# Kernel optimization log

Hardware: AMD Instinct MI355X
Metric: run time of the kernel (lower is better)

## Reference

```python
import jax, jax.numpy as jnp
import numpy as np

B, L, D_IN = 4, 2048, 80
D, H, DFF, WIN = 128, 16, 128, 64
DH = D // H
BN_EPS = 1e-5


def sinusoidal_positional_encoding(l, d, dtype):
    # Faithful to source: pos_j = 10000 ** (j / d) (exponent j/d, not 2j/d)
    n = d // 2 + (d % 2 == 1)
    pos_i = jnp.arange(l, dtype=dtype)[:, None]                  # [L,1]
    pos_j = jnp.power(jnp.asarray(10000.0, dtype), jnp.arange(n, dtype=dtype) / d)  # [n]
    ang = pos_i / pos_j                                          # [L,n]
    pos = jnp.stack([jnp.sin(ang), jnp.cos(ang)], axis=-1).reshape(l, -1)
    return pos[:, :d]                                            # [L,D]


def local_window_disallowed_mask(l, win):
    # Source: mask starts as ones (True = disallowed), zeros only strictly
    i = jnp.arange(l)
    diff = jnp.abs(i[:, None] - i[None, :])
    allowed = (diff >= 1) & (diff <= win)
    return ~allowed                                              # [L,L] bool, True = masked


def setup_inputs() -> dict:
    key = jax.random.key(0)
    ks = jax.random.split(key, 17)
    s = 0.05  # weight scale for numerical stability
    return {
        "x": jax.random.normal(ks[0], (B, L, D_IN), jnp.float32),
        "conv_w": jax.random.normal(ks[1], (D, D_IN), jnp.float32) * s,
        "conv_b": jax.random.normal(ks[2], (D,), jnp.float32) * s,
        "bn_g": jax.random.uniform(ks[3], (D,), jnp.float32, 0.5, 1.5),
        "bn_b": jax.random.normal(ks[4], (D,), jnp.float32) * s,
        "bn_rm": jax.random.normal(ks[5], (D,), jnp.float32) * s,
        "bn_rv": jax.random.uniform(ks[6], (D,), jnp.float32, 0.5, 1.5),
        "in_proj_w": jax.random.normal(ks[7], (3 * D, D), jnp.float32) * s,
        "in_proj_b": jax.random.normal(ks[8], (3 * D,), jnp.float32) * s,
        "out_w": jax.random.normal(ks[9], (D, D), jnp.float32) * s,
        "out_b": jax.random.normal(ks[10], (D,), jnp.float32) * s,
        "ff_w1": jax.random.normal(ks[11], (DFF, D), jnp.float32) * s,
        "ff_b1": jax.random.normal(ks[12], (DFF,), jnp.float32) * s,
        "ff_w2": jax.random.normal(ks[13], (D, DFF), jnp.float32) * s,
        "ff_b2": jax.random.normal(ks[14], (D,), jnp.float32) * s,
        "fc_w": jax.random.normal(ks[15], (D_IN, D), jnp.float32) * s,
        "fc_b": jax.random.normal(ks[16], (D_IN,), jnp.float32) * s,
    }


def _forward(x, conv_w, conv_b, bn_g, bn_b, bn_rm, bn_rv,
             in_proj_w, in_proj_b, out_w, out_b,
             ff_w1, ff_b1, ff_w2, ff_b2, fc_w, fc_b):
    b, l, _ = x.shape
    dt = x.dtype
    # Conv1d(kernel=1) + ReLU + BatchNorm1d (eval mode, running stats)
    h = jax.nn.relu(jnp.einsum('bli,oi->blo', x, conv_w) + conv_b)     # [B,L,D]
    h = (h - bn_rm) * (bn_g * jax.lax.rsqrt(bn_rv + BN_EPS)) + bn_b
    # positional encoding
    h = h + sinusoidal_positional_encoding(l, D, dt)
    # MultiheadAttention (torch semantics: joint in_proj, scaled dot, out_proj)
    qkv = jnp.einsum('bld,ed->ble', h, in_proj_w) + in_proj_b          # [B,L,3D]
    q, k, v = jnp.split(qkv, 3, axis=-1)
    q = q.reshape(b, l, H, DH).transpose(0, 2, 1, 3)                   # [B,H,L,dh]
    k = k.reshape(b, l, H, DH).transpose(0, 2, 1, 3)
    v = v.reshape(b, l, H, DH).transpose(0, 2, 1, 3)
    scores = jnp.einsum('bhqd,bhkd->bhqk', q, k) / jnp.sqrt(jnp.asarray(DH, dt))
    mask = local_window_disallowed_mask(l, WIN)                        # True = masked
    scores = jnp.where(mask, jnp.finfo(dt).min, scores)
    attn = jax.nn.softmax(scores, axis=-1)                             # [B,H,L,L]
    ctx = jnp.einsum('bhqk,bhkd->bhqd', attn, v)
    ctx = ctx.transpose(0, 2, 1, 3).reshape(b, l, D)
    attn_out = jnp.einsum('bld,od->blo', ctx, out_w) + out_b           # [B,L,D]
    # FFN (no residual in source)
    f = jax.nn.relu(jnp.einsum('bld,fd->blf', attn_out, ff_w1) + ff_b1)
    f = jnp.einsum('blf,df->bld', f, ff_w2) + ff_b2                    # [B,L,D]
    # final head
    return jnp.einsum('bld,od->blo', f, fc_w) + fc_b                   # [B,L,80]


def reference(x, conv_w, conv_b, bn_g, bn_b, bn_rm, bn_rv,
              in_proj_w, in_proj_b, out_w, out_b,
              ff_w1, ff_b1, ff_w2, ff_b2, fc_w, fc_b):
    return _forward(x, conv_w, conv_b, bn_g, bn_b, bn_rm, bn_rv,
                    in_proj_w, in_proj_b, out_w, out_b,
                    ff_w1, ff_b1, ff_w2, ff_b2, fc_w, fc_b)
```

## Files before the change

kernel.cpp:

```cpp
#include <hip/hip_runtime.h>
#include <math.h>

constexpr int L_ = 2048, D_ = 128, H_ = 16;
constexpr int T_ = 8192;
constexpr int DIN = 80;
constexpr int LDX = T_;
constexpr int BHL = 131072;

typedef __attribute__((ext_vector_type(8))) short short8;
typedef __attribute__((ext_vector_type(4))) float floatx4;

__device__ float g_xT  [DIN * T_];
__device__ float g_posT[D_ * L_];
__device__ unsigned short g_h_hi[T_ * D_];
__device__ unsigned short g_h_lo[T_ * D_];
__device__ unsigned short g_Wq_hi[3 * D_ * D_];
__device__ unsigned short g_Wq_lo[3 * D_ * D_];
__device__ float g_qkv [3 * D_ * T_];
__device__ float g_ctx [D_ * T_];
__device__ float g_f1  [D_ * T_];
__device__ float g_pA  [2 * 8 * BHL];
__device__ float g_pl  [2 * BHL];
__device__ float g_WconvT[DIN * D_];
__device__ float g_Wf1T  [D_ * D_];
__device__ float g_WfcT  [D_ * D_];
__device__ float g_bf1   [D_];
__device__ float g_bfc   [D_];

__device__ __forceinline__ unsigned short bf16h(float x) {
    unsigned u = __float_as_uint(x);
    return (unsigned short)((u + 0x7FFFu + ((u >> 16) & 1u)) >> 16);
}
__device__ __forceinline__ float bf16f(unsigned short h) {
    return __uint_as_float(((unsigned)h) << 16);
}

__global__ __launch_bounds__(256) void prep_kernel(
        const float* __restrict__ x,
        const float* __restrict__ conv_w,
        const float* __restrict__ in_proj_w,
        const float* __restrict__ out_w,  const float* __restrict__ out_b,
        const float* __restrict__ ff_w1,  const float* __restrict__ ff_b1,
        const float* __restrict__ ff_w2,  const float* __restrict__ ff_b2,
        const float* __restrict__ fc_w,   const float* __restrict__ fc_b) {
    __shared__ float smem[80 * 65];
    int bid = blockIdx.x, tid = threadIdx.x;

    if (bid < 128) {
        int t0 = bid * 64;
        for (int i = tid; i < 64 * 80; i += 256) {
            int t = i / 80, k = i - t * 80;
            smem[k * 65 + t] = x[(size_t)t0 * 80 + i];
        }
        __syncthreads();
        for (int i = tid; i < 80 * 64; i += 256) {
            int k = i >> 6, tt = i & 63;
            g_xT[(size_t)k * T_ + t0 + tt] = smem[k * 65 + tt];
        }
        return;
    }
    if (bid < 640) {
        int idx = (bid - 128) * 256 + tid;
        int l = idx >> 6, j = idx & 63;
        float inv = __expf((float)j * (-9.210340371976184f / 128.0f));
        float ang = (float)l * inv;
        g_posT[(2 * j) * L_ + l]     = sinf(ang);
        g_posT[(2 * j + 1) * L_ + l] = cosf(ang);
        return;
    }
    if (bid < 680) {
        int e = (bid - 640) * 256 + tid;
        int o = e / 80, k = e - o * 80;
        g_WconvT[k * D_ + o] = conv_w[e];
        return;
    }
    if (bid < 872) {
        int e = (bid - 680) * 256 + tid;
        float v = in_proj_w[e];
        unsigned short hi = bf16h(v);
        g_Wq_hi[e] = hi;
        g_Wq_lo[e] = bf16h(v - bf16f(hi));
        return;
    }
    float* rowbuf = smem;
    float* red = smem + 256;
    if (bid < 936) {
        int sub = tid >> 7, k = tid & 127;
        int f = (bid - 872) * 2 + sub;
        rowbuf[sub * 128 + k] = ff_w1[f * 128 + k];
        __syncthreads();
        float acc = 0.f;
#pragma unroll 8
        for (int o = 0; o < 128; o++)
            acc = fmaf(rowbuf[sub * 128 + o], out_w[o * 128 + k], acc);
        g_Wf1T[k * 128 + f] = acc;
        red[tid] = rowbuf[sub * 128 + k] * out_b[k];
        __syncthreads();
        for (int s = 64; s > 0; s >>= 1) {
            if (k < s) red[tid] += red[tid + s];
            __syncthreads();
        }
        if (k == 0) g_bf1[f] = red[sub * 128] + ff_b1[f];
        return;
    }
    {
        int sub = tid >> 7, k = tid & 127;
        int o = (bid - 936) * 2 + sub;
        rowbuf[sub * 128 + k] = (o < 80) ? fc_w[o * 128 + k] : 0.f;
        __syncthreads();
        float acc = 0.f;
#pragma unroll 8
        for (int d = 0; d < 128; d++)
            acc = fmaf(rowbuf[sub * 128 + d], ff_w2[d * 128 + k], acc);
        g_WfcT[k * 128 + o] = acc;
        red[tid] = rowbuf[sub * 128 + k] * ff_b2[k];
        __syncthreads();
        for (int s = 64; s > 0; s >>= 1) {
            if (k < s) red[tid] += red[tid + s];
            __syncthreads();
        }
        if (k == 0) g_bfc[o] = (o < 80) ? (red[sub * 128] + fc_b[o]) : 0.f;
        return;
    }
}

template <int K, int BK, int BN, int LDW, int EPI>
__global__ __launch_bounds__(256) void gemm_kernel(
        const float* __restrict__ X, const float* __restrict__ Wt,
        const float* __restrict__ bias,
        const float* __restrict__ bg, const float* __restrict__ bb,
        const float* __restrict__ brm, const float* __restrict__ brv,
        float* __restrict__ Y) {
    constexpr int TN = BN / 16;
    __shared__ float Xs[BK][64];
    __shared__ float Ws[BK][BN];
    int tid = threadIdx.x;
    int t0 = blockIdx.x * 64;
    int cb = blockIdx.y * BN;
    int tc = tid & 15, tr = tid >> 4;

    float acc[4][TN] = {};
    for (int kc = 0; kc < K; kc += BK) {
        for (int i = tid; i < BK * 16; i += 256) {
            int k = i >> 4, f = i & 15;
            *(float4*)&Xs[k][f * 4] =
                *(const float4*)&X[(size_t)(kc + k) * LDX + t0 + f * 4];
        }
        for (int i = tid; i < BK * (BN / 4); i += 256) {
            int k = i / (BN / 4), f = i - k * (BN / 4);
            *(float4*)&Ws[k][f * 4] =
                *(const float4*)&Wt[(size_t)(kc + k) * LDW + cb + f * 4];
        }
        __syncthreads();
#pragma unroll 4
        for (int k = 0; k < BK; ++k) {
            float4 a = *(float4*)&Xs[k][tr * 4];
            float av[4] = {a.x, a.y, a.z, a.w};
            float wv[TN];
#pragma unroll
            for (int jj = 0; jj < TN; jj++) wv[jj] = Ws[k][tc * TN + jj];
#pragma unroll
            for (int i = 0; i < 4; i++)
#pragma unroll
                for (int jj = 0; jj < TN; jj++)
                    acc[i][jj] = fmaf(av[i], wv[jj], acc[i][jj]);
        }
        __syncthreads();
    }

    if (EPI == 5) {
#pragma unroll
        for (int i = 0; i < 4; i++) {
            int t = t0 + tr * 4 + i;
            unsigned hi2 = 0, lo2 = 0;
#pragma unroll
            for (int jj = 0; jj < TN; jj++) {
                int c = cb + tc * TN + jj;
                float v = acc[i][jj] + bias[c];
                v = fmaxf(v, 0.0f);
                v = (v - brm[c]) * (bg[c] * rsqrtf(brv[c] + 1e-5f)) + bb[c];
                v += g_posT[c * L_ + (t & 2047)];
                unsigned short h = bf16h(v);
                float lo = v - bf16f(h);
                hi2 |= ((unsigned)h) << (16 * jj);
                lo2 |= ((unsigned)bf16h(lo)) << (16 * jj);
            }
            int cbase = cb + tc * TN;
            *(unsigned*)&g_h_hi[(size_t)t * 128 + cbase] = hi2;
            *(unsigned*)&g_h_lo[(size_t)t * 128 + cbase] = lo2;
        }
        return;
    }
    if (EPI == 4) {
#pragma unroll
        for (int jj = 0; jj < TN; jj++) {
            int c = cb + tc * TN + jj;
            if (c < 80) {
                float bv = bias[c];
#pragma unroll
                for (int i = 0; i < 4; i++) {
                    int t = t0 + tr * 4 + i;
                    Y[(size_t)t * 80 + c] = acc[i][jj] + bv;
                }
            }
        }
        return;
    }
#pragma unroll
    for (int jj = 0; jj < TN; jj++) {
        int c = cb + tc * TN + jj;
        float bv = bias[c];
        float vs[4];
#pragma unroll
        for (int i = 0; i < 4; i++) {
            float v = acc[i][jj] + bv;
            if (EPI == 1) v = fmaxf(v, 0.0f);
            vs[i] = v;
        }
        *(float4*)&Y[(size_t)c * LDX + t0 + tr * 4] = *(float4*)vs;
    }
}

__global__ __launch_bounds__(256) void qkv_mfma(const float* __restrict__ in_proj_b) {
    __shared__ unsigned short WsH[64 * 136];
    __shared__ unsigned short WsL[64 * 136];
    __shared__ unsigned short HsH[32 * 136];
    __shared__ unsigned short HsL[32 * 136];
    int tid = threadIdx.x;
    int t0 = blockIdx.x * 32;
    int cb = blockIdx.y * 64;

    for (int i = tid; i < 1024; i += 256) {
        int r = i >> 4, c8 = (i & 15) * 8;
        *(uint4*)&WsH[r * 136 + c8] = *(const uint4*)&g_Wq_hi[(size_t)(cb + r) * 128 + c8];
        *(uint4*)&WsL[r * 136 + c8] = *(const uint4*)&g_Wq_lo[(size_t)(cb + r) * 128 + c8];
    }
    for (int i = tid; i < 512; i += 256) {
        int r = i >> 4, c8 = (i & 15) * 8;
        *(uint4*)&HsH[r * 136 + c8] = *(const uint4*)&g_h_hi[(size_t)(t0 + r) * 128 + c8];
        *(uint4*)&HsL[r * 136 + c8] = *(const uint4*)&g_h_lo[(size_t)(t0 + r) * 128 + c8];
    }
    __syncthreads();

    int lane = tid & 63, w = tid >> 6;
    int m16 = lane & 15, quad = lane >> 4;
    int c0 = w * 16;

    short8 aH[4], aL[4];
#pragma unroll
    for (int kt = 0; kt < 4; kt++) {
        aH[kt] = *(short8*)&WsH[(c0 + m16) * 136 + kt * 32 + quad * 8];
        aL[kt] = *(short8*)&WsL[(c0 + m16) * 136 + kt * 32 + quad * 8];
    }
    float bias_r[4];
#pragma unroll
    for (int r = 0; r < 4; r++) bias_r[r] = in_proj_b[cb + c0 + quad * 4 + r];

#pragma unroll
    for (int s = 0; s < 2; s++) {
        floatx4 acc = {0.f, 0.f, 0.f, 0.f};
        int trow = s * 16 + m16;
#pragma unroll
        for (int kt = 0; kt < 4; kt++) {
            short8 bH = *(short8*)&HsH[trow * 136 + kt * 32 + quad * 8];
            short8 bL = *(short8*)&HsL[trow * 136 + kt * 32 + quad * 8];
            acc = __builtin_amdgcn_mfma_f32_16x16x32_bf16(aH[kt], bH, acc, 0, 0, 0);
            acc = __builtin_amdgcn_mfma_f32_16x16x32_bf16(aL[kt], bH, acc, 0, 0, 0);
            acc = __builtin_amdgcn_mfma_f32_16x16x32_bf16(aH[kt], bL, acc, 0, 0, 0);
        }
#pragma unroll
        for (int r = 0; r < 4; r++)
            g_qkv[(size_t)(cb + c0 + quad * 4 + r) * LDX + t0 + s * 16 + m16] =
                acc[r] + bias_r[r];
    }
}

__global__ __launch_bounds__(128) void attn_kernel() {
    __shared__ float4 SK[2][2][160];
    __shared__ float4 SV[2][2][160];
    int bh = blockIdx.x, tile = blockIdx.y, hf = blockIdx.z;
    int b = bh >> 4, h = bh & 15;
    int qb = tile * 256;
    int tid = threadIdx.x;
    int jbase = hf ? (qb + 1) : (qb - 64);
    int tb = b * L_;

    for (int c16 = 0; c16 < 16; c16++) {
        int d = c16 & 7;
        int ch = ((c16 < 8) ? D_ : 2 * D_) + h * 8 + d;
        const float* src = g_qkv + (size_t)ch * LDX + tb;
        for (int s = tid; s < 319; s += 128) {
            int j = jbase + s;
            float v = ((unsigned)j < (unsigned)L_) ? src[j] : 0.f;
            float4* arr = (c16 < 8) ? &SK[s & 1][d >> 2][s >> 1]
                                    : &SV[s & 1][d >> 2][s >> 1];
            ((float*)arr)[d & 3] = v;
        }
    }
    __syncthreads();

    const float sc = 0.35355339059327373f;
    int q0 = qb + 2 * tid;
    float qa[8], qc[8];
#pragma unroll
    for (int d = 0; d < 8; d++) {
        qa[d] = g_qkv[(size_t)(h * 8 + d) * LDX + tb + q0] * sc;
        qc[d] = g_qkv[(size_t)(h * 8 + d) * LDX + tb + q0 + 1] * sc;
    }

    float l0 = 0.f, l1 = 0.f;
    float A0[8] = {}, A1[8] = {};
    int j00 = jbase + 2 * tid;

    auto step = [&](int it, bool m0, bool m1) {
        int p = it & 1, idx = tid + (it >> 1);
        float4 ka = SK[p][0][idx], kb = SK[p][1][idx];
        float kv[8] = {ka.x, ka.y, ka.z, ka.w, kb.x, kb.y, kb.z, kb.w};
        float s0 = 0.f, s1 = 0.f;
#pragma unroll
        for (int d = 0; d < 8; d++) {
            s0 = fmaf(qa[d], kv[d], s0);
            s1 = fmaf(qc[d], kv[d], s1);
        }
        bool jv = (unsigned)(j00 + it) < (unsigned)L_;
        float w0 = (m0 && jv) ? __expf(s0) : 0.f;
        float w1 = (m1 && jv) ? __expf(s1) : 0.f;
        l0 += w0; l1 += w1;
        float4 va = SV[p][0][idx], vb = SV[p][1][idx];
        float vv[8] = {va.x, va.y, va.z, va.w, vb.x, vb.y, vb.z, vb.w};
#pragma unroll
        for (int d = 0; d < 8; d++) {
            A0[d] = fmaf(w0, vv[d], A0[d]);
            A1[d] = fmaf(w1, vv[d], A1[d]);
        }
    };

    step(0, true, false);
#pragma unroll 2
    for (int it = 1; it <= 63; it++) step(it, true, true);
    step(64, false, true);

    int base = bh * L_ + q0;
#pragma unroll
    for (int d = 0; d < 8; d++) {
        g_pA[(size_t)(hf * 8 + d) * BHL + base]     = A0[d];
        g_pA[(size_t)(hf * 8 + d) * BHL + base + 1] = A1[d];
    }
    g_pl[hf * BHL + base]     = l0;
    g_pl[hf * BHL + base + 1] = l1;
}

__global__ __launch_bounds__(256) void combine_kernel() {
    int gq = blockIdx.x * 256 + threadIdx.x;
    int bh = gq >> 11, l = gq & 2047;
    int b = bh >> 4, h = bh & 15;
    float inv = 1.f / (g_pl[gq] + g_pl[BHL + gq]);
#pragma unroll
    for (int d = 0; d < 8; d++) {
        float v = (g_pA[(size_t)d * BHL + gq] + g_pA[(size_t)(8 + d) * BHL + gq]) * inv;
        g_ctx[(size_t)(h * 8 + d) * LDX + b * L_ + l] = v;
    }
}

extern "C" void kernel_launch(void* const* d_in, const int* in_sizes, int n_in,
                              void* d_out, int out_size, void* d_ws, size_t ws_size,
                              hipStream_t stream) {
    const float* x         = (const float*)d_in[0];
    const float* conv_w    = (const float*)d_in[1];
    const float* conv_b    = (const float*)d_in[2];
    const float* bn_g      = (const float*)d_in[3];
    const float* bn_b      = (const float*)d_in[4];
    const float* bn_rm     = (const float*)d_in[5];
    const float* bn_rv     = (const float*)d_in[6];
    const float* in_proj_w = (const float*)d_in[7];
    const float* in_proj_b = (const float*)d_in[8];
    const float* out_w     = (const float*)d_in[9];
    const float* out_b     = (const float*)d_in[10];
    const float* ff_w1     = (const float*)d_in[11];
    const float* ff_b1     = (const float*)d_in[12];
    const float* ff_w2     = (const float*)d_in[13];
    const float* ff_b2     = (const float*)d_in[14];
    const float* fc_w      = (const float*)d_in[15];
    const float* fc_b      = (const float*)d_in[16];

    float *p_xT, *p_WconvT, *p_ctx, *p_f1, *p_Wf1T, *p_WfcT, *p_bf1, *p_bfc;
    hipGetSymbolAddress((void**)&p_xT,     HIP_SYMBOL(g_xT));
    hipGetSymbolAddress((void**)&p_WconvT, HIP_SYMBOL(g_WconvT));
    hipGetSymbolAddress((void**)&p_ctx,    HIP_SYMBOL(g_ctx));
    hipGetSymbolAddress((void**)&p_f1,     HIP_SYMBOL(g_f1));
    hipGetSymbolAddress((void**)&p_Wf1T,   HIP_SYMBOL(g_Wf1T));
    hipGetSymbolAddress((void**)&p_WfcT,   HIP_SYMBOL(g_WfcT));
    hipGetSymbolAddress((void**)&p_bf1,    HIP_SYMBOL(g_bf1));
    hipGetSymbolAddress((void**)&p_bfc,    HIP_SYMBOL(g_bfc));

    prep_kernel<<<1000, 256, 0, stream>>>(x, conv_w, in_proj_w, out_w, out_b,
                                          ff_w1, ff_b1, ff_w2, ff_b2, fc_w, fc_b);

    gemm_kernel<80, 80, 32, 128, 5><<<dim3(128, 4), 256, 0, stream>>>(
        p_xT, p_WconvT, conv_b, bn_g, bn_b, bn_rm, bn_rv, nullptr);

    qkv_mfma<<<dim3(256, 6), 256, 0, stream>>>(in_proj_b);

    attn_kernel<<<dim3(64, 8, 2), 128, 0, stream>>>();
    combine_kernel<<<512, 256, 0, stream>>>();

    gemm_kernel<128, 128, 32, 128, 1><<<dim3(128, 4), 256, 0, stream>>>(
        p_ctx, p_Wf1T, p_bf1, nullptr, nullptr, nullptr, nullptr, p_f1);

    gemm_kernel<128, 128, 32, 128, 4><<<dim3(128, 3), 256, 0, stream>>>(
        p_f1, p_WfcT, p_bfc, nullptr, nullptr, nullptr, nullptr, (float*)d_out);
}
```

Measured before the change: 163.2 us.

## Fuse attention halves, drop combine pass, fuse FFN and head into one MFMA kernel

The attention kernel now processes the full 129-key window per query pair in one 256-thread block instead of splitting it into two halves plus a separate combine kernel. It normalises in place and writes the context as split bf16 hi/lo in token-major layout. The two trailing FP32 SIMT GEMMs (FFN first layer and fused FFN2+head) become a single MFMA kernel using a three-term bf16 hi/lo split, keeping the intermediate in shared memory. This removes two launches and the partial-sum and intermediate global round trips. The cost is extra MFMA work for split precision and a longer serial loop per attention thread.

Result: faster. 154.7 us (-5.2%).

```diff
diff --git a/kernel.cpp b/kernel.cpp
--- a/kernel.cpp
+++ b/kernel.cpp
@@ -5,7 +5,6 @@
 constexpr int T_ = 8192;
 constexpr int DIN = 80;
 constexpr int LDX = T_;
-constexpr int BHL = 131072;
 
 typedef __attribute__((ext_vector_type(8))) short short8;
 typedef __attribute__((ext_vector_type(4))) float floatx4;
@@ -17,13 +16,13 @@
 __device__ unsigned short g_Wq_hi[3 * D_ * D_];
 __device__ unsigned short g_Wq_lo[3 * D_ * D_];
 __device__ float g_qkv [3 * D_ * T_];
-__device__ float g_ctx [D_ * T_];
-__device__ float g_f1  [D_ * T_];
-__device__ float g_pA  [2 * 8 * BHL];
-__device__ float g_pl  [2 * BHL];
+__device__ unsigned short g_ctxH[T_ * D_];
+__device__ unsigned short g_ctxL[T_ * D_];
+__device__ unsigned short g_Mf1H[D_ * D_];
+__device__ unsigned short g_Mf1L[D_ * D_];
+__device__ unsigned short g_MfcH[D_ * D_];
+__device__ unsigned short g_MfcL[D_ * D_];
 __device__ float g_WconvT[DIN * D_];
-__device__ float g_Wf1T  [D_ * D_];
-__device__ float g_WfcT  [D_ * D_];
 __device__ float g_bf1   [D_];
 __device__ float g_bfc   [D_];
 
@@ -93,7 +92,9 @@
 #pragma unroll 8
         for (int o = 0; o < 128; o++)
             acc = fmaf(rowbuf[sub * 128 + o], out_w[o * 128 + k], acc);
-        g_Wf1T[k * 128 + f] = acc;
+        unsigned short hi = bf16h(acc);
+        g_Mf1H[f * 128 + k] = hi;
+        g_Mf1L[f * 128 + k] = bf16h(acc - bf16f(hi));
         red[tid] = rowbuf[sub * 128 + k] * out_b[k];
         __syncthreads();
         for (int s = 64; s > 0; s >>= 1) {
@@ -112,7 +113,9 @@
 #pragma unroll 8
         for (int d = 0; d < 128; d++)
             acc = fmaf(rowbuf[sub * 128 + d], ff_w2[d * 128 + k], acc);
-        g_WfcT[k * 128 + o] = acc;
+        unsigned short hi = bf16h(acc);
+        g_MfcH[o * 128 + k] = hi;
+        g_MfcL[o * 128 + k] = bf16h(acc - bf16f(hi));
         red[tid] = rowbuf[sub * 128 + k] * ff_b2[k];
         __syncthreads();
         for (int s = 64; s > 0; s >>= 1) {
@@ -124,14 +127,12 @@
     }
 }
 
-template <int K, int BK, int BN, int LDW, int EPI>
-__global__ __launch_bounds__(256) void gemm_kernel(
+__global__ __launch_bounds__(256) void conv_kernel(
         const float* __restrict__ X, const float* __restrict__ Wt,
         const float* __restrict__ bias,
         const float* __restrict__ bg, const float* __restrict__ bb,
-        const float* __restrict__ brm, const float* __restrict__ brv,
-        float* __restrict__ Y) {
-    constexpr int TN = BN / 16;
+        const float* __restrict__ brm, const float* __restrict__ brv) {
+    constexpr int BK = 80, BN = 32, TN = 2;
     __shared__ float Xs[BK][64];
     __shared__ float Ws[BK][BN];
     int tid = threadIdx.x;
@@ -140,84 +141,50 @@
     int tc = tid & 15, tr = tid >> 4;
 
     float acc[4][TN] = {};
-    for (int kc = 0; kc < K; kc += BK) {
-        for (int i = tid; i < BK * 16; i += 256) {
-            int k = i >> 4, f = i & 15;
-            *(float4*)&Xs[k][f * 4] =
-                *(const float4*)&X[(size_t)(kc + k) * LDX + t0 + f * 4];
-        }
-        for (int i = tid; i < BK * (BN / 4); i += 256) {
-            int k = i / (BN / 4), f = i - k * (BN / 4);
-            *(float4*)&Ws[k][f * 4] =
-                *(const float4*)&Wt[(size_t)(kc + k) * LDW + cb + f * 4];
-        }
-        __syncthreads();
+    for (int i = tid; i < BK * 16; i += 256) {
+        int k = i >> 4, f = i & 15;
+        *(float4*)&Xs[k][f * 4] =
+            *(const float4*)&X[(size_t)k * LDX + t0 + f * 4];
+    }
+    for (int i = tid; i < BK * (BN / 4); i += 256) {
+        int k = i / (BN / 4), f = i - k * (BN / 4);
+        *(float4*)&Ws[k][f * 4] =
+            *(const float4*)&Wt[(size_t)k * D_ + cb + f * 4];
+    }
+    __syncthreads();
 #pragma unroll 4
-        for (int k = 0; k < BK; ++k) {
-            float4 a = *(float4*)&Xs[k][tr * 4];
-            float av[4] = {a.x, a.y, a.z, a.w};
-            float wv[TN];
-#pragma unroll
-            for (int jj = 0; jj < TN; jj++) wv[jj] = Ws[k][tc * TN + jj];
-#pragma unroll
-            for (int i = 0; i < 4; i++)
-#pragma unroll
-                for (int jj = 0; jj < TN; jj++)
-                    acc[i][jj] = fmaf(av[i], wv[jj], acc[i][jj]);
-        }
-        __syncthreads();
-    }
-
-    if (EPI == 5) {
-#pragma unroll
-        for (int i = 0; i < 4; i++) {
-            int t = t0 + tr * 4 + i;
-            unsigned hi2 = 0, lo2 = 0;
-#pragma unroll
-            for (int jj = 0; jj < TN; jj++) {
-                int c = cb + tc * TN + jj;
-                float v = acc[i][jj] + bias[c];
-                v = fmaxf(v, 0.0f);
-                v = (v - brm[c]) * (bg[c] * rsqrtf(brv[c] + 1e-5f)) + bb[c];
-                v += g_posT[c * L_ + (t & 2047)];
-                unsigned short h = bf16h(v);
-                float lo = v - bf16f(h);
-                hi2 |= ((unsigned)h) << (16 * jj);
-                lo2 |= ((unsigned)bf16h(lo)) << (16 * jj);
-            }
-            int cbase = cb + tc * TN;
-            *(unsigned*)&g_h_hi[(size_t)t * 128 + cbase] = hi2;
-            *(unsigned*)&g_h_lo[(size_t)t * 128 + cbase] = lo2;
-        }
-        return;
-    }
-    if (EPI == 4) {
+    for (int k = 0; k < BK; ++k) {
+        float4 a = *(float4*)&Xs[k][tr * 4];
+        float av[4] = {a.x, a.y, a.z, a.w};
+        float wv[TN];
+#pragma unroll
+        for (int jj = 0; jj < TN; jj++) wv[jj] = Ws[k][tc * TN + jj];
+#pragma unroll
+        for (int i = 0; i < 4; i++)
+#pragma unroll
+            for (int jj = 0; jj < TN; jj++)
+                acc[i][jj] = fmaf(av[i], wv[jj], acc[i][jj]);
+    }
+
+#pragma unroll
+    for (int i = 0; i < 4; i++) {
+        int t = t0 + tr * 4 + i;
+        unsigned hi2 = 0, lo2 = 0;
 #pragma unroll
         for (int jj = 0; jj < TN; jj++) {
             int c = cb + tc * TN + jj;
-            if (c < 80) {
-                float bv = bias[c];
-#pragma unroll
-                for (int i = 0; i < 4; i++) {
-                    int t = t0 + tr * 4 + i;
-                    Y[(size_t)t * 80 + c] = acc[i][jj] + bv;
-                }
-            }
-        }
-        return;
-    }
-#pragma unroll
-    for (int jj = 0; jj < TN; jj++) {
-        int c = cb + tc * TN + jj;
-        float bv = bias[c];
-        float vs[4];
-#pragma unroll
-        for (int i = 0; i < 4; i++) {
-            float v = acc[i][jj] + bv;
-            if (EPI == 1) v = fmaxf(v, 0.0f);
-            vs[i] = v;
-        }
-        *(float4*)&Y[(size_t)c * LDX + t0 + tr * 4] = *(float4*)vs;
+            float v = acc[i][jj] + bias[c];
+            v = fmaxf(v, 0.0f);
+            v = (v - brm[c]) * (bg[c] * rsqrtf(brv[c] + 1e-5f)) + bb[c];
+            v += g_posT[c * L_ + (t & 2047)];
+            unsigned short h = bf16h(v);
+            float lo = v - bf16f(h);
+            hi2 |= ((unsigned)h) << (16 * jj);
+            lo2 |= ((unsigned)bf16h(lo)) << (16 * jj);
+        }
+        int cbase = cb + tc * TN;
+        *(unsigned*)&g_h_hi[(size_t)t * 128 + cbase] = hi2;
+        *(unsigned*)&g_h_lo[(size_t)t * 128 + cbase] = lo2;
     }
 }
 
@@ -275,26 +242,25 @@
     }
 }
 
-__global__ __launch_bounds__(128) void attn_kernel() {
-    __shared__ float4 SK[2][2][160];
-    __shared__ float4 SV[2][2][160];
-    int bh = blockIdx.x, tile = blockIdx.y, hf = blockIdx.z;
+__global__ __launch_bounds__(256) void attn_kernel() {
+    __shared__ float4 SK[2][2][324];
+    __shared__ float4 SV[2][2][324];
+    int bh = blockIdx.x;
+    int qb = blockIdx.y * 512;
     int b = bh >> 4, h = bh & 15;
-    int qb = tile * 256;
+    int tb = b * L_;
     int tid = threadIdx.x;
-    int jbase = hf ? (qb + 1) : (qb - 64);
-    int tb = b * L_;
+    int jbase = qb - 64;
 
     for (int c16 = 0; c16 < 16; c16++) {
         int d = c16 & 7;
         int ch = ((c16 < 8) ? D_ : 2 * D_) + h * 8 + d;
         const float* src = g_qkv + (size_t)ch * LDX + tb;
-        for (int s = tid; s < 319; s += 128) {
+        float4* base4 = ((c16 < 8) ? &SK[0][0][0] : &SV[0][0][0]) + (d >> 2) * 324;
+        for (int s = tid; s < 641; s += 256) {
             int j = jbase + s;
             float v = ((unsigned)j < (unsigned)L_) ? src[j] : 0.f;
-            float4* arr = (c16 < 8) ? &SK[s & 1][d >> 2][s >> 1]
-                                    : &SV[s & 1][d >> 2][s >> 1];
-            ((float*)arr)[d & 3] = v;
+            ((float*)(base4 + (s & 1) * 648 + (s >> 1)))[d & 3] = v;
         }
     }
     __syncthreads();
@@ -307,15 +273,15 @@
         qa[d] = g_qkv[(size_t)(h * 8 + d) * LDX + tb + q0] * sc;
         qc[d] = g_qkv[(size_t)(h * 8 + d) * LDX + tb + q0 + 1] * sc;
     }
-
     float l0 = 0.f, l1 = 0.f;
     float A0[8] = {}, A1[8] = {};
     int j00 = jbase + 2 * tid;
 
-    auto step = [&](int it, bool m0, bool m1) {
-        int p = it & 1, idx = tid + (it >> 1);
-        float4 ka = SK[p][0][idx], kb = SK[p][1][idx];
-        float kv[8] = {ka.x, ka.y, ka.z, ka.w, kb.x, kb.y, kb.z, kb.w};
+#pragma unroll 2
+    for (int it = 0; it <= 129; it++) {
+        int pp = it & 1, idx = tid + (it >> 1);
+        float4 ka = SK[pp][0][idx], kb2 = SK[pp][1][idx];
+        float kv[8] = {ka.x, ka.y, ka.z, ka.w, kb2.x, kb2.y, kb2.z, kb2.w};
         float s0 = 0.f, s1 = 0.f;
 #pragma unroll
         for (int d = 0; d < 8; d++) {
@@ -323,42 +289,154 @@
             s1 = fmaf(qc[d], kv[d], s1);
         }
         bool jv = (unsigned)(j00 + it) < (unsigned)L_;
-        float w0 = (m0 && jv) ? __expf(s0) : 0.f;
-        float w1 = (m1 && jv) ? __expf(s1) : 0.f;
+        float w0 = (jv && it != 64 && it <= 128) ? __expf(s0) : 0.f;
+        float w1 = (jv && it != 65 && it >= 1)  ? __expf(s1) : 0.f;
         l0 += w0; l1 += w1;
-        float4 va = SV[p][0][idx], vb = SV[p][1][idx];
-        float vv[8] = {va.x, va.y, va.z, va.w, vb.x, vb.y, vb.z, vb.w};
+        float4 va = SV[pp][0][idx], vb2 = SV[pp][1][idx];
+        float vv[8] = {va.x, va.y, va.z, va.w, vb2.x, vb2.y, vb2.z, vb2.w};
 #pragma unroll
         for (int d = 0; d < 8; d++) {
             A0[d] = fmaf(w0, vv[d], A0[d]);
             A1[d] = fmaf(w1, vv[d], A1[d]);
         }
-    };
-
-    step(0, true, false);
-#pragma unroll 2
-    for (int it = 1; it <= 63; it++) step(it, true, true);
-    step(64, false, true);
-
-    int base = bh * L_ + q0;
-#pragma unroll
-    for (int d = 0; d < 8; d++) {
-        g_pA[(size_t)(hf * 8 + d) * BHL + base]     = A0[d];
-        g_pA[(size_t)(hf * 8 + d) * BHL + base + 1] = A1[d];
-    }
-    g_pl[hf * BHL + base]     = l0;
-    g_pl[hf * BHL + base + 1] = l1;
-}
-
-__global__ __launch_bounds__(256) void combine_kernel() {
-    int gq = blockIdx.x * 256 + threadIdx.x;
-    int bh = gq >> 11, l = gq & 2047;
-    int b = bh >> 4, h = bh & 15;
-    float inv = 1.f / (g_pl[gq] + g_pl[BHL + gq]);
-#pragma unroll
-    for (int d = 0; d < 8; d++) {
-        float v = (g_pA[(size_t)d * BHL + gq] + g_pA[(size_t)(8 + d) * BHL + gq]) * inv;
-        g_ctx[(size_t)(h * 8 + d) * LDX + b * L_ + l] = v;
+    }
+    float i0 = 1.f / l0, i1 = 1.f / l1;
+    unsigned hp[4], lp[4];
+#pragma unroll
+    for (int d2 = 0; d2 < 4; d2++) {
+        float v0 = A0[2 * d2] * i0, v1 = A0[2 * d2 + 1] * i0;
+        unsigned short h0 = bf16h(v0), h1 = bf16h(v1);
+        hp[d2] = (unsigned)h0 | ((unsigned)h1 << 16);
+        lp[d2] = (unsigned)bf16h(v0 - bf16f(h0)) |
+                 ((unsigned)bf16h(v1 - bf16f(h1)) << 16);
+    }
+    *(uint4*)&g_ctxH[(size_t)(tb + q0) * 128 + h * 8] = *(uint4*)hp;
+    *(uint4*)&g_ctxL[(size_t)(tb + q0) * 128 + h * 8] = *(uint4*)lp;
+#pragma unroll
+    for (int d2 = 0; d2 < 4; d2++) {
+        float v0 = A1[2 * d2] * i1, v1 = A1[2 * d2 + 1] * i1;
+        unsigned short h0 = bf16h(v0), h1 = bf16h(v1);
+        hp[d2] = (unsigned)h0 | ((unsigned)h1 << 16);
+        lp[d2] = (unsigned)bf16h(v0 - bf16f(h0)) |
+                 ((unsigned)bf16h(v1 - bf16f(h1)) << 16);
+    }
+    *(uint4*)&g_ctxH[(size_t)(tb + q0 + 1) * 128 + h * 8] = *(uint4*)hp;
+    *(uint4*)&g_ctxL[(size_t)(tb + q0 + 1) * 128 + h * 8] = *(uint4*)lp;
+}
+
+__global__ __launch_bounds__(256) void f1fc_mfma(float* __restrict__ out) {
+    __shared__ unsigned short sm[4 * 32 * 136];
+    unsigned short* ctxH = sm;
+    unsigned short* ctxL = sm + 32 * 136;
+    unsigned short* C1H  = sm + 2 * 32 * 136;
+    unsigned short* C1L  = sm + 3 * 32 * 136;
+    float* C2 = (float*)sm;
+    __shared__ float b1s[128];
+
+    int tid = threadIdx.x;
+    int t0 = blockIdx.x * 32;
+
+    for (int i = tid; i < 512; i += 256) {
+        int r = i >> 4, c8 = (i & 15) * 8;
+        *(uint4*)&ctxH[r * 136 + c8] = *(const uint4*)&g_ctxH[(size_t)(t0 + r) * 128 + c8];
+        *(uint4*)&ctxL[r * 136 + c8] = *(const uint4*)&g_ctxL[(size_t)(t0 + r) * 128 + c8];
+    }
+    if (tid < 128) b1s[tid] = g_bf1[tid];
+    __syncthreads();
+
+    int lane = tid & 63, w = tid >> 6;
+    int m16 = lane & 15, quad = lane >> 4;
+
+    floatx4 acc1[2][2];
+#pragma unroll
+    for (int mt = 0; mt < 2; mt++) {
+        int fbase = w * 32 + mt * 16 + m16;
+        short8 aH[4], aL[4];
+#pragma unroll
+        for (int kt = 0; kt < 4; kt++) {
+            aH[kt] = *(const short8*)&g_Mf1H[(size_t)fbase * 128 + kt * 32 + quad * 8];
+            aL[kt] = *(const short8*)&g_Mf1L[(size_t)fbase * 128 + kt * 32 + quad * 8];
+        }
+#pragma unroll
+        for (int nt = 0; nt < 2; nt++) {
+            floatx4 acc = {0.f, 0.f, 0.f, 0.f};
+            int trow = nt * 16 + m16;
+#pragma unroll
+            for (int kt = 0; kt < 4; kt++) {
+                short8 bH = *(short8*)&ctxH[trow * 136 + kt * 32 + quad * 8];
+                short8 bL = *(short8*)&ctxL[trow * 136 + kt * 32 + quad * 8];
+                acc = __builtin_amdgcn_mfma_f32_16x16x32_bf16(aH[kt], bH, acc, 0, 0, 0);
+                acc = __builtin_amdgcn_mfma_f32_16x16x32_bf16(aL[kt], bH, acc, 0, 0, 0);
+                acc = __builtin_amdgcn_mfma_f32_16x16x32_bf16(aH[kt], bL, acc, 0, 0, 0);
+            }
+            acc1[mt][nt] = acc;
+        }
+    }
+#pragma unroll
+    for (int mt = 0; mt < 2; mt++) {
+#pragma unroll
+        for (int nt = 0; nt < 2; nt++) {
+            int f0 = w * 32 + mt * 16 + quad * 4;
+            int t = nt * 16 + m16;
+            float v[4];
+#pragma unroll
+            for (int r = 0; r < 4; r++)
+                v[r] = fmaxf(acc1[mt][nt][r] + b1s[f0 + r], 0.f);
+            unsigned short h0 = bf16h(v[0]), h1 = bf16h(v[1]);
+            unsigned short h2 = bf16h(v[2]), h3 = bf16h(v[3]);
+            *(unsigned*)&C1H[t * 136 + f0]     = (unsigned)h0 | ((unsigned)h1 << 16);
+            *(unsigned*)&C1H[t * 136 + f0 + 2] = (unsigned)h2 | ((unsigned)h3 << 16);
+            *(unsigned*)&C1L[t * 136 + f0] =
+                (unsigned)bf16h(v[0] - bf16f(h0)) | ((unsigned)bf16h(v[1] - bf16f(h1)) << 16);
+            *(unsigned*)&C1L[t * 136 + f0 + 2] =
+                (unsigned)bf16h(v[2] - bf16f(h2)) | ((unsigned)bf16h(v[3] - bf16f(h3)) << 16);
+        }
+    }
+    __syncthreads();
+
+    floatx4 acc2[2][2];
+#pragma unroll
+    for (int mt = 0; mt < 2; mt++) {
+        int obase = w * 32 + mt * 16 + m16;
+        short8 aH[4], aL[4];
+#pragma unroll
+        for (int kt = 0; kt < 4; kt++) {
+            aH[kt] = *(const short8*)&g_MfcH[(size_t)obase * 128 + kt * 32 + quad * 8];
+            aL[kt] = *(const short8*)&g_MfcL[(size_t)obase * 128 + kt * 32 + quad * 8];
+        }
+#pragma unroll
+        for (int nt = 0; nt < 2; nt++) {
+            floatx4 acc = {0.f, 0.f, 0.f, 0.f};
+            int trow = nt * 16 + m16;
+#pragma unroll
+            for (int kt = 0; kt < 4; kt++) {
+                short8 bH = *(short8*)&C1H[trow * 136 + kt * 32 + quad * 8];
+                short8 bL = *(short8*)&C1L[trow * 136 + kt * 32 + quad * 8];
+                acc = __builtin_amdgcn_mfma_f32_16x16x32_bf16(aH[kt], bH, acc, 0, 0, 0);
+                acc = __builtin_amdgcn_mfma_f32_16x16x32_bf16(aL[kt], bH, acc, 0, 0, 0);
+                acc = __builtin_amdgcn_mfma_f32_16x16x32_bf16(aH[kt], bL, acc, 0, 0, 0);
+            }
+            acc2[mt][nt] = acc;
+        }
+    }
+    __syncthreads();
+#pragma unroll
+    for (int mt = 0; mt < 2; mt++) {
+        int o0 = w * 32 + mt * 16 + quad * 4;
+        if (o0 < 96) {
+#pragma unroll
+            for (int nt = 0; nt < 2; nt++) {
+                int t = nt * 16 + m16;
+#pragma unroll
+                for (int r = 0; r < 4; r++)
+                    C2[t * 100 + o0 + r] = acc2[mt][nt][r] + g_bfc[o0 + r];
+            }
+        }
+    }
+    __syncthreads();
+    for (int i = tid; i < 640; i += 256) {
+        int t = i / 20, c4 = i - t * 20;
+        *(float4*)&out[(size_t)(t0 + t) * 80 + c4 * 4] = *(float4*)&C2[t * 100 + c4 * 4];
     }
 }
 
@@ -383,30 +461,19 @@
     const float* fc_w      = (const float*)d_in[15];
     const float* fc_b      = (const float*)d_in[16];
 
-    float *p_xT, *p_WconvT, *p_ctx, *p_f1, *p_Wf1T, *p_WfcT, *p_bf1, *p_bfc;
+    float *p_xT, *p_WconvT;
     hipGetSymbolAddress((void**)&p_xT,     HIP_SYMBOL(g_xT));
     hipGetSymbolAddress((void**)&p_WconvT, HIP_SYMBOL(g_WconvT));
-    hipGetSymbolAddress((void**)&p_ctx,    HIP_SYMBOL(g_ctx));
-    hipGetSymbolAddress((void**)&p_f1,     HIP_SYMBOL(g_f1));
-    hipGetSymbolAddress((void**)&p_Wf1T,   HIP_SYMBOL(g_Wf1T));
-    hipGetSymbolAddress((void**)&p_WfcT,   HIP_SYMBOL(g_WfcT));
-    hipGetSymbolAddress((void**)&p_bf1,    HIP_SYMBOL(g_bf1));
-    hipGetSymbolAddress((void**)&p_bfc,    HIP_SYMBOL(g_bfc));
 
     prep_kernel<<<1000, 256, 0, stream>>>(x, conv_w, in_proj_w, out_w, out_b,
                                           ff_w1, ff_b1, ff_w2, ff_b2, fc_w, fc_b);
 
-    gemm_kernel<80, 80, 32, 128, 5><<<dim3(128, 4), 256, 0, stream>>>(
-        p_xT, p_WconvT, conv_b, bn_g, bn_b, bn_rm, bn_rv, nullptr);
+    conv_kernel<<<dim3(128, 4), 256, 0, stream>>>(
+        p_xT, p_WconvT, conv_b, bn_g, bn_b, bn_rm, bn_rv);
 
     qkv_mfma<<<dim3(256, 6), 256, 0, stream>>>(in_proj_b);
 
-    attn_kernel<<<dim3(64, 8, 2), 128, 0, stream>>>();
-    combine_kernel<<<512, 256, 0, stream>>>();
-
-    gemm_kernel<128, 128, 32, 128, 1><<<dim3(128, 4), 256, 0, stream>>>(
-        p_ctx, p_Wf1T, p_bf1, nullptr, nullptr, nullptr, nullptr, p_f1);
-
-    gemm_kernel<128, 128, 32, 128, 4><<<dim3(128, 3), 256, 0, stream>>>(
-        p_f1, p_WfcT, p_bfc, nullptr, nullptr, nullptr, nullptr, (float*)d_out);
-}
+    attn_kernel<<<dim3(64, 4), 256, 0, stream>>>();
+
+    f1fc_mfma<<<256, 256, 0, stream>>>((float*)d_out);
+}
```
